# Kernel optimization log

Measured on AMD Instinct MI355X. Metric: run time of the kernel, lower is better.

The kernel has to match this reference:

```python
import jax, jax.numpy as jnp
import numpy as np

N_NODES = 100000
N_EDGES = 1600000
N_GRAPHS = 64
C_IN = 64
HID = 64
N_CLASSES = 10
EPS = 1e-5


def setup_inputs() -> dict:
    key = jax.random.key(0)
    ks = jax.random.split(key, 12)
    x = jax.random.normal(ks[0], (N_NODES, C_IN), dtype=jnp.float32)
    edge_index = jax.random.randint(ks[1], (2, N_EDGES), 0, N_NODES, dtype=jnp.int64)
    batch = jnp.sort(jax.random.randint(ks[2], (N_NODES,), 0, N_GRAPHS, dtype=jnp.int64))

    def lin(k, fan_in, fan_out):
        lim = 1.0 / np.sqrt(fan_in)
        kw, kb = jax.random.split(k)
        W = jax.random.uniform(kw, (fan_in, fan_out), minval=-lim, maxval=lim, dtype=jnp.float32)
        b = jax.random.uniform(kb, (fan_out,), minval=-lim, maxval=lim, dtype=jnp.float32)
        return W, b

    W1, b1 = lin(ks[3], 2 * C_IN, HID)
    W2, b2 = lin(ks[4], 2 * HID, HID)
    W3, b3 = lin(ks[5], 2 * HID, HID)
    Wo, bo = lin(ks[6], HID, N_CLASSES)
    g1 = jnp.ones((HID,), jnp.float32); be1 = jnp.zeros((HID,), jnp.float32)
    g2 = jnp.ones((HID,), jnp.float32); be2 = jnp.zeros((HID,), jnp.float32)
    g3 = jnp.ones((HID,), jnp.float32); be3 = jnp.zeros((HID,), jnp.float32)
    return {"x": x, "edge_index": edge_index, "batch": batch,
            "W1": W1, "b1": b1, "W2": W2, "b2": b2, "W3": W3, "b3": b3,
            "g1": g1, "be1": be1, "g2": g2, "be2": be2, "g3": g3, "be3": be3,
            "Wo": Wo, "bo": bo}


def edge_conv(x, src, dst, W, b):
    # PyG EdgeConv: message = mlp(cat([x_i, x_j - x_i])), aggr = max over incoming edges
    xi = x[dst]                       # target node feats [E, C]
    xj = x[src]                       # source node feats [E, C]
    m = jax.nn.relu(jnp.concatenate([xi, xj - xi], axis=-1) @ W + b)  # [E, H]
    out = jax.ops.segment_max(m, dst, num_segments=N_NODES)
    return jnp.where(jnp.isfinite(out), out, 0.0)  # nodes with no edges -> 0


def batch_norm(x, g, b):
    # training-mode BatchNorm1d over node axis, biased variance
    mu = jnp.mean(x, axis=0)
    var = jnp.mean(jnp.square(x - mu), axis=0)
    return (x - mu) * jax.lax.rsqrt(var + EPS) * g + b


def reference(x, edge_index, batch, W1, b1, W2, b2, W3, b3,
              g1, be1, g2, be2, g3, be3, Wo, bo):
    src, dst = edge_index[0], edge_index[1]
    h = edge_conv(x, src, dst, W1, b1)
    h = jax.nn.relu(batch_norm(h, g1, be1))
    h = edge_conv(h, src, dst, W2, b2)
    h = jax.nn.relu(batch_norm(h, g2, be2))
    h = edge_conv(h, src, dst, W3, b3)
    h = batch_norm(h, g3, be3)
    # global mean pool over graphs
    sums = jax.ops.segment_sum(h, batch, num_segments=N_GRAPHS)        # [G, H]
    cnts = jax.ops.segment_sum(jnp.ones((h.shape[0],), h.dtype), batch, num_segments=N_GRAPHS)
    pooled = sums / jnp.maximum(cnts, 1.0)[:, None]
    logits = pooled @ Wo + bo
    return jax.nn.softmax(logits, axis=1)
```

## Files before the change

kernel.cpp:

```cpp
#include <hip/hip_runtime.h>
#include <hip/hip_bf16.h>
#include <math.h>

#define N_NODES 100000
#define N_EDGES 1600000
#define N_GRAPHS 64
#define EPS 1e-5f
#define NBUCK 391
#define EBLK 782
#define BSCAT_GRID 196
#define SEG_NBLK 3125
#define GEMM_TILES 1563

typedef unsigned int u32;
typedef __attribute__((ext_vector_type(8))) short short8;
typedef __attribute__((ext_vector_type(4))) float f32x4;

static __device__ __forceinline__ ushort f2bf(float f) {
  u32 x = __float_as_uint(f);
  u32 r = (x + 0x7fffu + ((x >> 16) & 1u)) >> 16;
  return (ushort)r;
}
static __device__ __forceinline__ float bflo(u32 w) { return __uint_as_float(w << 16); }
static __device__ __forceinline__ float bfhi(u32 w) { return __uint_as_float(w & 0xffff0000u); }
static __device__ __forceinline__ void decode8(uint4 w, float* f) {
  f[0] = bflo(w.x); f[1] = bfhi(w.x); f[2] = bflo(w.y); f[3] = bfhi(w.y);
  f[4] = bflo(w.z); f[5] = bfhi(w.z); f[6] = bflo(w.w); f[7] = bfhi(w.w);
}

__global__ __launch_bounds__(256) void setup_k(
    const int* __restrict__ dst, u32* __restrict__ bcnt,
    const float* __restrict__ W1, const float* __restrict__ W2,
    const float* __restrict__ W3, uint4* __restrict__ Wb,
    const int* __restrict__ batch, u32* __restrict__ bounds,
    u32* __restrict__ zbase) {
  __shared__ u32 csh[NBUCK];
  int bid = blockIdx.x, t = threadIdx.x;
  if (bid < EBLK) {
    for (int i = t; i < NBUCK; i += 256) csh[i] = 0;
    __syncthreads();
    int base = bid * 2048;
#pragma unroll
    for (int k = 0; k < 8; ++k) {
      int e = base + k * 256 + t;
      if (e < N_EDGES) atomicAdd(&csh[(u32)dst[e] >> 8], 1u);
    }
    __syncthreads();
    for (int i = t; i < NBUCK; i += 256) {
      u32 cc = csh[i];
      if (cc) atomicAdd(&bcnt[i], cc);
    }
  } else if (bid < EBLK + 12) {
    int g = (bid - EBLK) * 256 + t;
    if (g >= 3072) return;
    int layer = g >> 10, rem = g & 1023;
    int kh = rem >> 9, ct = (rem >> 6) & 7, l = rem & 63;
    const float* W = (layer == 0) ? W1 : (layer == 1) ? W2 : W3;
    int c = ct * 16 + (l & 15);
    u32 w[4];
#pragma unroll
    for (int jj = 0; jj < 4; ++jj) {
      int k0 = kh * 32 + (l >> 4) * 8 + 2 * jj;
      float v0, v1;
      if (c < 64) {
        v0 = W[k0 * 64 + c] - W[(64 + k0) * 64 + c];
        v1 = W[(k0 + 1) * 64 + c] - W[(65 + k0) * 64 + c];
      } else {
        v0 = W[(64 + k0) * 64 + (c - 64)];
        v1 = W[(65 + k0) * 64 + (c - 64)];
      }
      w[jj] = (u32)f2bf(v0) | ((u32)f2bf(v1) << 16);
    }
    Wb[g] = make_uint4(w[0], w[1], w[2], w[3]);
  } else if (bid == EBLK + 12) {
    if (t > 64) return;
    int lo = 0, hi = N_NODES;
    while (lo < hi) {
      int mid = (lo + hi) >> 1;
      if (batch[mid] < t) lo = mid + 1; else hi = mid;
    }
    bounds[t] = (u32)lo;
  } else {
    for (int i = t; i < 16448; i += 256) zbase[i] = 0u;
  }
}

__global__ void bscan_k(const u32* __restrict__ bcnt, u32* __restrict__ boffs,
                        u32* __restrict__ bcur) {
  __shared__ u32 s[512];
  int t = threadIdx.x;
  u32 v = (t < NBUCK) ? bcnt[t] : 0u;
  s[t] = v;
  __syncthreads();
  for (int d = 1; d < 512; d <<= 1) {
    u32 a = (t >= d) ? s[t - d] : 0u;
    __syncthreads();
    s[t] += a;
    __syncthreads();
  }
  if (t < NBUCK) { boffs[t] = s[t] - v; bcur[t] = s[t] - v; }
  if (t == NBUCK - 1) boffs[NBUCK] = s[t];
}

__global__ __launch_bounds__(256) void bscat_k(const int* __restrict__ src,
                                               const int* __restrict__ dst,
                                               u32* __restrict__ gcur,
                                               u32* __restrict__ pairs) {
  __shared__ u32 cnt[NBUCK];
  __shared__ u32 base[NBUCK];
  int t = threadIdx.x;
  for (int i = t; i < NBUCK; i += 256) cnt[i] = 0;
  __syncthreads();
  u32 pk[32], bk[32];
  int be = blockIdx.x * 8192;
#pragma unroll
  for (int k = 0; k < 32; ++k) {
    int e = be + k * 256 + t;
    if (e < N_EDGES) {
      u32 d = (u32)dst[e], s = (u32)src[e];
      u32 b = d >> 8;
      pk[k] = ((d & 255u) << 24) | s;
      bk[k] = b;
      atomicAdd(&cnt[b], 1u);
    } else bk[k] = 0xFFFFFFFFu;
  }
  __syncthreads();
  for (int i = t; i < NBUCK; i += 256) {
    u32 c = cnt[i];
    base[i] = c ? atomicAdd(&gcur[i], c) : 0u;
    cnt[i] = 0;
  }
  __syncthreads();
#pragma unroll
  for (int k = 0; k < 32; ++k) {
    if (bk[k] != 0xFFFFFFFFu) {
      u32 p = base[bk[k]] + atomicAdd(&cnt[bk[k]], 1u);
      pairs[p] = pk[k];
    }
  }
}

static __device__ __forceinline__ void fscat2_body(
    int b, u32* SH, const u32* __restrict__ boffs, const u32* __restrict__ pairs,
    u32* __restrict__ esrc, u32* __restrict__ offs_g, u32* __restrict__ cnt_g) {
  u32* lcnt = SH; u32* lexc = SH + 256; u32* lcur = SH + 512;
  int t = threadIdx.x;
  u32 s0 = boffs[b], e0 = boffs[b + 1];
  lcnt[t] = 0;
  __syncthreads();
  for (u32 p = s0 + t; p < e0; p += 256) atomicAdd(&lcnt[pairs[p] >> 24], 1u);
  __syncthreads();
  u32 v = lcnt[t];
  lexc[t] = v;
  __syncthreads();
  for (int d = 1; d < 256; d <<= 1) {
    u32 a = (t >= d) ? lexc[t - d] : 0u;
    __syncthreads();
    lexc[t] += a;
    __syncthreads();
  }
  u32 excl = lexc[t] - v;
  int node = (b << 8) + t;
  if (node < N_NODES) { offs_g[node] = s0 + excl; cnt_g[node] = v; }
  lcur[t] = 0;
  lexc[t] = excl;
  __syncthreads();
  for (u32 p = s0 + t; p < e0; p += 256) {
    u32 pk = pairs[p];
    u32 dl = pk >> 24;
    u32 l = atomicAdd(&lcur[dl], 1u);
    esrc[s0 + lexc[dl] + l] = pk & 0x00FFFFFFu;
  }
}

static __device__ __forceinline__ void gemm_body(
    int tile, u32* Xl,
    const void* __restrict__ xin, int xbf16, const uint4* __restrict__ Wb,
    const float* ab, const float* __restrict__ bias,
    ushort* __restrict__ ub, ushort* __restrict__ vb) {
  int t = threadIdx.x;
  int l = t & 63, wv = t >> 6;
  short8 bs[2][8];
#pragma unroll
  for (int kh = 0; kh < 2; ++kh)
#pragma unroll
    for (int ct = 0; ct < 8; ++ct) {
      uint4 tmp = Wb[(kh * 8 + ct) * 64 + l];
      __builtin_memcpy(&bs[kh][ct], &tmp, 16);
    }
  int srow = t >> 2, scol = (t & 3) * 16;
  int rb = tile * 64;
  int gr = rb + srow;
  u32 xb[8];
  if (gr < N_NODES) {
    if (xbf16) {
      const uint4* xp = (const uint4*)((const ushort*)xin + (size_t)gr * 64 + scol);
      uint4 p0 = xp[0], p1 = xp[1];
      u32 raw[8] = {p0.x, p0.y, p0.z, p0.w, p1.x, p1.y, p1.z, p1.w};
#pragma unroll
      for (int q = 0; q < 8; ++q) {
        int c = scol + 2 * q;
        float lo = fmaxf(fmaf(bflo(raw[q]), ab[c], ab[64 + c]), 0.f);
        float hi = fmaxf(fmaf(bfhi(raw[q]), ab[c + 1], ab[64 + c + 1]), 0.f);
        xb[q] = (u32)f2bf(lo) | ((u32)f2bf(hi) << 16);
      }
    } else {
      const float4* xp = (const float4*)((const float*)xin + (size_t)gr * 64 + scol);
#pragma unroll
      for (int q = 0; q < 4; ++q) {
        float4 a = xp[q];
        xb[2 * q]     = (u32)f2bf(a.x) | ((u32)f2bf(a.y) << 16);
        xb[2 * q + 1] = (u32)f2bf(a.z) | ((u32)f2bf(a.w) << 16);
      }
    }
  } else {
#pragma unroll
    for (int q = 0; q < 8; ++q) xb[q] = 0u;
  }
  int byte0 = srow * 128 + ((scol * 2) ^ ((srow & 7) << 4));
  int byte1 = srow * 128 + ((scol * 2 + 16) ^ ((srow & 7) << 4));
  *(uint4*)((char*)Xl + byte0) = make_uint4(xb[0], xb[1], xb[2], xb[3]);
  *(uint4*)((char*)Xl + byte1) = make_uint4(xb[4], xb[5], xb[6], xb[7]);
  __syncthreads();
  f32x4 acc[8];
#pragma unroll
  for (int ct = 0; ct < 8; ++ct) {
    float b0 = (ct < 4) ? bias[ct * 16 + (l & 15)] : 0.f;
    acc[ct] = (f32x4){b0, b0, b0, b0};
  }
  int arow = wv * 16 + (l & 15);
#pragma unroll
  for (int kh = 0; kh < 2; ++kh) {
    int abyte = arow * 128 + ((kh * 64 + ((l >> 4) * 16)) ^ ((arow & 7) << 4));
    short8 af = *(const short8*)((const char*)Xl + abyte);
#pragma unroll
    for (int ct = 0; ct < 8; ++ct)
      acc[ct] = __builtin_amdgcn_mfma_f32_16x16x32_bf16(af, bs[kh][ct], acc[ct], 0, 0, 0);
  }
  int rloc = rb + wv * 16 + 4 * (l >> 4);
#pragma unroll
  for (int ct = 0; ct < 4; ++ct) {
    int col = ct * 16 + (l & 15);
#pragma unroll
    for (int r = 0; r < 4; ++r) {
      int row = rloc + r;
      if (row < N_NODES) ub[(size_t)row * 64 + col] = f2bf(acc[ct][r]);
    }
  }
#pragma unroll
  for (int ct = 4; ct < 8; ++ct) {
    int col = ct * 16 + (l & 15) - 64;
#pragma unroll
    for (int r = 0; r < 4; ++r) {
      int row = rloc + r;
      if (row < N_NODES) vb[(size_t)row * 64 + col] = f2bf(acc[ct][r]);
    }
  }
}

__global__ __launch_bounds__(256) void fused_fg_k(
    const u32* __restrict__ boffs, const u32* __restrict__ pairs,
    u32* __restrict__ esrc, u32* __restrict__ offs_g, u32* __restrict__ cnt_g,
    const float* __restrict__ x, const uint4* __restrict__ Wb,
    const float* __restrict__ bias, ushort* __restrict__ ub, ushort* __restrict__ vb) {
  __shared__ u32 SH[2048];
  int bid = blockIdx.x;
  if (bid < NBUCK) fscat2_body(bid, SH, boffs, pairs, esrc, offs_g, cnt_g);
  else gemm_body(bid - NBUCK, SH, x, 0, Wb, nullptr, bias, ub, vb);
}

__global__ __launch_bounds__(256) void gemm_k(
    const ushort* __restrict__ xin, const uint4* __restrict__ Wb,
    const float* __restrict__ bnacc, const float* __restrict__ g,
    const float* __restrict__ be, const float* __restrict__ bias,
    ushort* __restrict__ ub, ushort* __restrict__ vb) {
  __shared__ u32 Xl[2048];
  __shared__ float ab_sh[128];
  int t = threadIdx.x;
  if (t < 64) {
    float s1 = 0.f, s2 = 0.f;
    for (int s = 0; s < 32; ++s) {
      s1 += bnacc[s * 128 + t];
      s2 += bnacc[s * 128 + 64 + t];
    }
    float mu = s1 / (float)N_NODES;
    float var = s2 / (float)N_NODES - mu * mu;
    float al = g[t] / sqrtf(var + EPS);
    ab_sh[t] = al;
    ab_sh[64 + t] = be[t] - mu * al;
  }
  __syncthreads();
  gemm_body(blockIdx.x, Xl, xin, 1, Wb, ab_sh, bias, ub, vb);
}

__global__ __launch_bounds__(256) void segmax_k(
    const ushort* __restrict__ v, const u32* __restrict__ offs,
    const u32* __restrict__ cnt, const u32* __restrict__ esrc,
    const ushort* __restrict__ ub, ushort* __restrict__ hb,
    float* __restrict__ bnacc) {
  int t = threadIdx.x;
  int lane = t & 63;
  int op = lane & 7;
  int sub = lane >> 3;
  int wv = t >> 6;
  int node = blockIdx.x * 32 + wv * 8 + sub;
  const uint4* v4 = (const uint4*)v;
  const uint4* u4 = (const uint4*)ub;
  uint4* h4 = (uint4*)hb;
  u32 off = offs[node], deg = cnt[node];
  const u32* ep = esrc + off;
  float m[8];
#pragma unroll
  for (int j = 0; j < 8; ++j) m[j] = -INFINITY;
  u32 i = 0;
  for (; i + 4 <= deg; i += 4) {
    u32 sA = ep[i], sB = ep[i + 1], sC = ep[i + 2], sD = ep[i + 3];
    uint4 wA = v4[(size_t)sA * 8 + op];
    uint4 wB = v4[(size_t)sB * 8 + op];
    uint4 wC = v4[(size_t)sC * 8 + op];
    uint4 wD = v4[(size_t)sD * 8 + op];
    float fA[8], fB[8], fC[8], fD[8];
    decode8(wA, fA); decode8(wB, fB); decode8(wC, fC); decode8(wD, fD);
#pragma unroll
    for (int j = 0; j < 8; ++j)
      m[j] = fmaxf(fmaxf(m[j], fmaxf(fA[j], fB[j])), fmaxf(fC[j], fD[j]));
  }
  for (; i < deg; ++i) {
    uint4 w = v4[(size_t)ep[i] * 8 + op];
    float f[8]; decode8(w, f);
#pragma unroll
    for (int j = 0; j < 8; ++j) m[j] = fmaxf(m[j], f[j]);
  }
  uint4 uu = u4[(size_t)node * 8 + op];
  float uf[8]; decode8(uu, uf);
  float h[8];
#pragma unroll
  for (int j = 0; j < 8; ++j) h[j] = fmaxf(uf[j] + m[j], 0.f);
  uint4 hw;
  hw.x = (u32)f2bf(h[0]) | ((u32)f2bf(h[1]) << 16);
  hw.y = (u32)f2bf(h[2]) | ((u32)f2bf(h[3]) << 16);
  hw.z = (u32)f2bf(h[4]) | ((u32)f2bf(h[5]) << 16);
  hw.w = (u32)f2bf(h[6]) | ((u32)f2bf(h[7]) << 16);
  h4[(size_t)node * 8 + op] = hw;
  __shared__ float red[2048];
#pragma unroll
  for (int j = 0; j < 8; ++j) red[t * 8 + j] = h[j];
  __syncthreads();
  float o1 = 0.f, o2 = 0.f;
  if (t < 64) {
    int cop = t >> 3, cj = t & 7;
    for (int q = 0; q < 32; ++q) o1 += red[(q * 8 + cop) * 8 + cj];
  }
  __syncthreads();
#pragma unroll
  for (int j = 0; j < 8; ++j) red[t * 8 + j] = h[j] * h[j];
  __syncthreads();
  if (t < 64) {
    int cop = t >> 3, cj = t & 7;
    for (int q = 0; q < 32; ++q) o2 += red[(q * 8 + cop) * 8 + cj];
    int slice = blockIdx.x & 31;
    atomicAdd(&bnacc[slice * 128 + t], o1);
    atomicAdd(&bnacc[slice * 128 + 64 + t], o2);
  }
}

__global__ __launch_bounds__(256) void pool_part_k(
    const ushort* __restrict__ h3, const u32* __restrict__ bounds,
    float* __restrict__ sums) {
  int g = blockIdx.y;
  u32 s = bounds[g], e = bounds[g + 1];
  int t = threadIdx.x;
  int op = t & 7;
  int slot = blockIdx.x * 32 + (t >> 3);
  int nsl = gridDim.x * 32;
  const uint4* h4 = (const uint4*)h3;
  float acc[8];
#pragma unroll
  for (int j = 0; j < 8; ++j) acc[j] = 0.f;
  for (u32 n = s + slot; n < e; n += nsl) {
    uint4 w = h4[(size_t)n * 8 + op];
    float f[8]; decode8(w, f);
#pragma unroll
    for (int j = 0; j < 8; ++j) acc[j] += f[j];
  }
  __shared__ float red[2048];
#pragma unroll
  for (int j = 0; j < 8; ++j) red[t * 8 + j] = acc[j];
  __syncthreads();
  if (t < 64) {
    int cop = t >> 3, cj = t & 7;
    float o = 0.f;
    for (int q = 0; q < 32; ++q) o += red[(q * 8 + cop) * 8 + cj];
    atomicAdd(&sums[g * 64 + t], o);
  }
}

__global__ void head_k(const float* __restrict__ sums, const u32* __restrict__ bounds,
                       const float* __restrict__ bnacc3, const float* __restrict__ g3,
                       const float* __restrict__ be3, const float* __restrict__ Wo,
                       const float* __restrict__ bo, float* __restrict__ out) {
  __shared__ float ab3[128];
  int t = threadIdx.x;
  if (t < 64) {
    float s1 = 0.f, s2 = 0.f;
    for (int sl = 0; sl < 32; ++sl) {
      s1 += bnacc3[sl * 128 + t];
      s2 += bnacc3[sl * 128 + 64 + t];
    }
    float mu = s1 / (float)N_NODES;
    float var = s2 / (float)N_NODES - mu * mu;
    float al = g3[t] / sqrtf(var + EPS);
    ab3[t] = al;
    ab3[64 + t] = be3[t] - mu * al;
  }
  __syncthreads();
  if (t >= N_GRAPHS) return;
  u32 cntn = bounds[t + 1] - bounds[t];
  float inv = (cntn > 0) ? 1.f / (float)cntn : 0.f;
  float lg[10];
#pragma unroll
  for (int j = 0; j < 10; ++j) lg[j] = bo[j];
  for (int c = 0; c < 64; ++c) {
    float p = (cntn > 0) ? (sums[t * 64 + c] * inv * ab3[c] + ab3[64 + c]) : 0.f;
#pragma unroll
    for (int j = 0; j < 10; ++j) lg[j] = fmaf(p, Wo[c * 10 + j], lg[j]);
  }
  float mx = lg[0];
#pragma unroll
  for (int j = 1; j < 10; ++j) mx = fmaxf(mx, lg[j]);
  float ssum = 0.f, ex[10];
#pragma unroll
  for (int j = 0; j < 10; ++j) { ex[j] = expf(lg[j] - mx); ssum += ex[j]; }
#pragma unroll
  for (int j = 0; j < 10; ++j) out[t * 10 + j] = ex[j] / ssum;
}

extern "C" void kernel_launch(void* const* d_in, const int* in_sizes, int n_in,
                              void* d_out, int out_size, void* d_ws, size_t ws_size,
                              hipStream_t stream) {
  const float* x    = (const float*)d_in[0];
  const int*   ei   = (const int*)d_in[1];
  const int*   batch= (const int*)d_in[2];
  const float* W1 = (const float*)d_in[3];  const float* b1 = (const float*)d_in[4];
  const float* W2 = (const float*)d_in[5];  const float* b2 = (const float*)d_in[6];
  const float* W3 = (const float*)d_in[7];  const float* b3 = (const float*)d_in[8];
  const float* g1 = (const float*)d_in[9];  const float* be1= (const float*)d_in[10];
  const float* g2 = (const float*)d_in[11]; const float* be2= (const float*)d_in[12];
  const float* g3 = (const float*)d_in[13]; const float* be3= (const float*)d_in[14];
  const float* Wo = (const float*)d_in[15]; const float* bo = (const float*)d_in[16];
  float* out = (float*)d_out;

  char* p = (char*)d_ws;
  auto alloc = [&](size_t bytes) { void* r = (void*)p; p += (bytes + 255) & ~(size_t)255; return r; };
  uint4* Wb     = (uint4*)alloc(3072 * sizeof(uint4));
  u32*   bounds = (u32*)alloc(65 * sizeof(u32));
  u32*   bcnt   = (u32*)alloc(NBUCK * sizeof(u32));
  u32*   boffs  = (u32*)alloc((NBUCK + 1) * sizeof(u32));
  u32*   bcur   = (u32*)alloc(NBUCK * sizeof(u32));
  u32*   cnt    = (u32*)alloc((size_t)N_NODES * sizeof(u32));
  u32*   offs   = (u32*)alloc((size_t)N_NODES * sizeof(u32));
  float* sums   = (float*)alloc(4096 * sizeof(float));
  float* bnacc  = (float*)alloc(12288 * sizeof(float));
  u32*   spare  = (u32*)alloc(256);
  (void)spare;
  u32*   esrc   = (u32*)alloc((size_t)N_EDGES * sizeof(u32));
  u32*   pairs  = (u32*)alloc((size_t)N_EDGES * sizeof(u32));
  ushort* ub    = (ushort*)alloc((size_t)N_NODES * 64 * sizeof(ushort));
  ushort* vb    = (ushort*)alloc((size_t)N_NODES * 64 * sizeof(ushort));
  ushort* hb    = (ushort*)alloc((size_t)N_NODES * 64 * sizeof(ushort));

  const int* src = ei;
  const int* dst = ei + N_EDGES;

  hipMemsetAsync(bcnt, 0, NBUCK * sizeof(u32), stream);
  setup_k<<<EBLK + 14, 256, 0, stream>>>(dst, bcnt, W1, W2, W3, Wb, batch, bounds,
                                         (u32*)sums);
  bscan_k<<<1, 512, 0, stream>>>(bcnt, boffs, bcur);
  bscat_k<<<BSCAT_GRID, 256, 0, stream>>>(src, dst, bcur, pairs);

  fused_fg_k<<<NBUCK + GEMM_TILES, 256, 0, stream>>>(boffs, pairs, esrc, offs, cnt,
                                                     x, Wb, b1, ub, vb);
  segmax_k<<<SEG_NBLK, 256, 0, stream>>>(vb, offs, cnt, esrc, ub, hb, bnacc);

  gemm_k<<<GEMM_TILES, 256, 0, stream>>>(hb, Wb + 1024, bnacc, g1, be1, b2, ub, vb);
  segmax_k<<<SEG_NBLK, 256, 0, stream>>>(vb, offs, cnt, esrc, ub, hb, bnacc + 4096);

  gemm_k<<<GEMM_TILES, 256, 0, stream>>>(hb, Wb + 2048, bnacc + 4096, g2, be2, b3, ub, vb);
  segmax_k<<<SEG_NBLK, 256, 0, stream>>>(vb, offs, cnt, esrc, ub, hb, bnacc + 8192);

  pool_part_k<<<dim3(16, N_GRAPHS), 256, 0, stream>>>(hb, bounds, sums);
  head_k<<<1, 64, 0, stream>>>(sums, bounds, bnacc + 8192, g3, be3, Wo, bo, out);
}
```

Measured before the change: 225.7 us.

## Replace bucket count-scan pass with fixed-stride bucket slots, dropping two kernels

Result: faster. 205.5 us (-9.0%).

```diff
diff --git a/kernel.cpp b/kernel.cpp
--- a/kernel.cpp
+++ b/kernel.cpp
@@ -7,7 +7,7 @@
 #define N_GRAPHS 64
 #define EPS 1e-5f
 #define NBUCK 391
-#define EBLK 782
+#define BSTRIDE 6144
 #define BSCAT_GRID 196
 #define SEG_NBLK 3125
 #define GEMM_TILES 1563
@@ -28,30 +28,48 @@
   f[4] = bflo(w.z); f[5] = bfhi(w.z); f[6] = bflo(w.w); f[7] = bfhi(w.w);
 }
 
-__global__ __launch_bounds__(256) void setup_k(
-    const int* __restrict__ dst, u32* __restrict__ bcnt,
+__global__ __launch_bounds__(256) void bscat_setup_k(
+    const int* __restrict__ src, const int* __restrict__ dst,
+    u32* __restrict__ bcur, u32* __restrict__ pairs,
     const float* __restrict__ W1, const float* __restrict__ W2,
     const float* __restrict__ W3, uint4* __restrict__ Wb,
     const int* __restrict__ batch, u32* __restrict__ bounds,
     u32* __restrict__ zbase) {
-  __shared__ u32 csh[NBUCK];
+  __shared__ u32 cnt[NBUCK];
+  __shared__ u32 base[NBUCK];
   int bid = blockIdx.x, t = threadIdx.x;
-  if (bid < EBLK) {
-    for (int i = t; i < NBUCK; i += 256) csh[i] = 0;
+  if (bid < BSCAT_GRID) {
+    for (int i = t; i < NBUCK; i += 256) cnt[i] = 0;
     __syncthreads();
-    int base = bid * 2048;
-#pragma unroll
-    for (int k = 0; k < 8; ++k) {
-      int e = base + k * 256 + t;
-      if (e < N_EDGES) atomicAdd(&csh[(u32)dst[e] >> 8], 1u);
+    u32 pk[32], bk[32];
+    int be = bid * 8192;
+#pragma unroll
+    for (int k = 0; k < 32; ++k) {
+      int e = be + k * 256 + t;
+      if (e < N_EDGES) {
+        u32 d = (u32)dst[e], s = (u32)src[e];
+        u32 b = d >> 8;
+        pk[k] = ((d & 255u) << 24) | s;
+        bk[k] = b;
+        atomicAdd(&cnt[b], 1u);
+      } else bk[k] = 0xFFFFFFFFu;
     }
     __syncthreads();
     for (int i = t; i < NBUCK; i += 256) {
-      u32 cc = csh[i];
-      if (cc) atomicAdd(&bcnt[i], cc);
-    }
-  } else if (bid < EBLK + 12) {
-    int g = (bid - EBLK) * 256 + t;
+      u32 c = cnt[i];
+      base[i] = c ? (i * BSTRIDE + atomicAdd(&bcur[i], c)) : 0u;
+      cnt[i] = 0;
+    }
+    __syncthreads();
+#pragma unroll
+    for (int k = 0; k < 32; ++k) {
+      if (bk[k] != 0xFFFFFFFFu) {
+        u32 p = base[bk[k]] + atomicAdd(&cnt[bk[k]], 1u);
+        pairs[p] = pk[k];
+      }
+    }
+  } else if (bid < BSCAT_GRID + 12) {
+    int g = (bid - BSCAT_GRID) * 256 + t;
     if (g >= 3072) return;
     int layer = g >> 10, rem = g & 1023;
     int kh = rem >> 9, ct = (rem >> 6) & 7, l = rem & 63;
@@ -72,7 +90,7 @@
       w[jj] = (u32)f2bf(v0) | ((u32)f2bf(v1) << 16);
     }
     Wb[g] = make_uint4(w[0], w[1], w[2], w[3]);
-  } else if (bid == EBLK + 12) {
+  } else if (bid == BSCAT_GRID + 12) {
     if (t > 64) return;
     int lo = 0, hi = N_NODES;
     while (lo < hi) {
@@ -85,67 +103,12 @@
   }
 }
 
-__global__ void bscan_k(const u32* __restrict__ bcnt, u32* __restrict__ boffs,
-                        u32* __restrict__ bcur) {
-  __shared__ u32 s[512];
-  int t = threadIdx.x;
-  u32 v = (t < NBUCK) ? bcnt[t] : 0u;
-  s[t] = v;
-  __syncthreads();
-  for (int d = 1; d < 512; d <<= 1) {
-    u32 a = (t >= d) ? s[t - d] : 0u;
-    __syncthreads();
-    s[t] += a;
-    __syncthreads();
-  }
-  if (t < NBUCK) { boffs[t] = s[t] - v; bcur[t] = s[t] - v; }
-  if (t == NBUCK - 1) boffs[NBUCK] = s[t];
-}
-
-__global__ __launch_bounds__(256) void bscat_k(const int* __restrict__ src,
-                                               const int* __restrict__ dst,
-                                               u32* __restrict__ gcur,
-                                               u32* __restrict__ pairs) {
-  __shared__ u32 cnt[NBUCK];
-  __shared__ u32 base[NBUCK];
-  int t = threadIdx.x;
-  for (int i = t; i < NBUCK; i += 256) cnt[i] = 0;
-  __syncthreads();
-  u32 pk[32], bk[32];
-  int be = blockIdx.x * 8192;
-#pragma unroll
-  for (int k = 0; k < 32; ++k) {
-    int e = be + k * 256 + t;
-    if (e < N_EDGES) {
-      u32 d = (u32)dst[e], s = (u32)src[e];
-      u32 b = d >> 8;
-      pk[k] = ((d & 255u) << 24) | s;
-      bk[k] = b;
-      atomicAdd(&cnt[b], 1u);
-    } else bk[k] = 0xFFFFFFFFu;
-  }
-  __syncthreads();
-  for (int i = t; i < NBUCK; i += 256) {
-    u32 c = cnt[i];
-    base[i] = c ? atomicAdd(&gcur[i], c) : 0u;
-    cnt[i] = 0;
-  }
-  __syncthreads();
-#pragma unroll
-  for (int k = 0; k < 32; ++k) {
-    if (bk[k] != 0xFFFFFFFFu) {
-      u32 p = base[bk[k]] + atomicAdd(&cnt[bk[k]], 1u);
-      pairs[p] = pk[k];
-    }
-  }
-}
-
 static __device__ __forceinline__ void fscat2_body(
-    int b, u32* SH, const u32* __restrict__ boffs, const u32* __restrict__ pairs,
+    int b, u32* SH, const u32* __restrict__ bcur, const u32* __restrict__ pairs,
     u32* __restrict__ esrc, u32* __restrict__ offs_g, u32* __restrict__ cnt_g) {
   u32* lcnt = SH; u32* lexc = SH + 256; u32* lcur = SH + 512;
   int t = threadIdx.x;
-  u32 s0 = boffs[b], e0 = boffs[b + 1];
+  u32 s0 = b * BSTRIDE, e0 = s0 + bcur[b];
   lcnt[t] = 0;
   __syncthreads();
   for (u32 p = s0 + t; p < e0; p += 256) atomicAdd(&lcnt[pairs[p] >> 24], 1u);
@@ -259,13 +222,13 @@
 }
 
 __global__ __launch_bounds__(256) void fused_fg_k(
-    const u32* __restrict__ boffs, const u32* __restrict__ pairs,
+    const u32* __restrict__ bcur, const u32* __restrict__ pairs,
     u32* __restrict__ esrc, u32* __restrict__ offs_g, u32* __restrict__ cnt_g,
     const float* __restrict__ x, const uint4* __restrict__ Wb,
     const float* __restrict__ bias, ushort* __restrict__ ub, ushort* __restrict__ vb) {
   __shared__ u32 SH[2048];
   int bid = blockIdx.x;
-  if (bid < NBUCK) fscat2_body(bid, SH, boffs, pairs, esrc, offs_g, cnt_g);
+  if (bid < NBUCK) fscat2_body(bid, SH, bcur, pairs, esrc, offs_g, cnt_g);
   else gemm_body(bid - NBUCK, SH, x, 0, Wb, nullptr, bias, ub, vb);
 }
 
@@ -454,17 +417,13 @@
   auto alloc = [&](size_t bytes) { void* r = (void*)p; p += (bytes + 255) & ~(size_t)255; return r; };
   uint4* Wb     = (uint4*)alloc(3072 * sizeof(uint4));
   u32*   bounds = (u32*)alloc(65 * sizeof(u32));
-  u32*   bcnt   = (u32*)alloc(NBUCK * sizeof(u32));
-  u32*   boffs  = (u32*)alloc((NBUCK + 1) * sizeof(u32));
   u32*   bcur   = (u32*)alloc(NBUCK * sizeof(u32));
   u32*   cnt    = (u32*)alloc((size_t)N_NODES * sizeof(u32));
   u32*   offs   = (u32*)alloc((size_t)N_NODES * sizeof(u32));
   float* sums   = (float*)alloc(4096 * sizeof(float));
   float* bnacc  = (float*)alloc(12288 * sizeof(float));
-  u32*   spare  = (u32*)alloc(256);
-  (void)spare;
-  u32*   esrc   = (u32*)alloc((size_t)N_EDGES * sizeof(u32));
-  u32*   pairs  = (u32*)alloc((size_t)N_EDGES * sizeof(u32));
+  u32*   esrc   = (u32*)alloc((size_t)NBUCK * BSTRIDE * sizeof(u32));
+  u32*   pairs  = (u32*)alloc((size_t)NBUCK * BSTRIDE * sizeof(u32));
   ushort* ub    = (ushort*)alloc((size_t)N_NODES * 64 * sizeof(ushort));
   ushort* vb    = (ushort*)alloc((size_t)N_NODES * 64 * sizeof(ushort));
   ushort* hb    = (ushort*)alloc((size_t)N_NODES * 64 * sizeof(ushort));
@@ -472,13 +431,12 @@
   const int* src = ei;
   const int* dst = ei + N_EDGES;
 
-  hipMemsetAsync(bcnt, 0, NBUCK * sizeof(u32), stream);
-  setup_k<<<EBLK + 14, 256, 0, stream>>>(dst, bcnt, W1, W2, W3, Wb, batch, bounds,
-                                         (u32*)sums);
-  bscan_k<<<1, 512, 0, stream>>>(bcnt, boffs, bcur);
-  bscat_k<<<BSCAT_GRID, 256, 0, stream>>>(src, dst, bcur, pairs);
-
-  fused_fg_k<<<NBUCK + GEMM_TILES, 256, 0, stream>>>(boffs, pairs, esrc, offs, cnt,
+  hipMemsetAsync(bcur, 0, NBUCK * sizeof(u32), stream);
+  bscat_setup_k<<<BSCAT_GRID + 14, 256, 0, stream>>>(src, dst, bcur, pairs,
+                                                     W1, W2, W3, Wb, batch, bounds,
+                                                     (u32*)sums);
+
+  fused_fg_k<<<NBUCK + GEMM_TILES, 256, 0, stream>>>(bcur, pairs, esrc, offs, cnt,
                                                      x, Wb, b1, ub, vb);
   segmax_k<<<SEG_NBLK, 256, 0, stream>>>(vb, offs, cnt, esrc, ub, hb, bnacc);
 
```
